# Kernel tuning notes

Measured on AMD Instinct MI355X. Metric: run time of the kernel, lower is better.

Reference implementation:

```python
import jax, jax.numpy as jnp
import numpy as np

D_MODEL = 256; D_FFN = 1024; N_LEVELS = 4; N_HEADS = 8; N_POINTS = 4; N_VT = 8
D_HEAD = D_MODEL // N_HEADS
SHAPES = [(64, 64), (32, 32), (16, 16), (8, 8)]
L_SP = sum(h * w for h, w in SHAPES)  # 5440
BATCH = 4
EPS = 1e-5


def _ln(x, g, b):
    m = jnp.mean(x, -1, keepdims=True)
    xc = x - m
    v = jnp.mean(xc * xc, -1, keepdims=True)
    return g * xc * jax.lax.rsqrt(v + EPS) + b


def _bilinear(v_flat, x, y, H, W):
    # v_flat: (N, H*W, M, Dh); x, y: (N, Q, M) pixel coords (align_corners=False, zero padding)
    x0 = jnp.floor(x); y0 = jnp.floor(y)
    wx = x - x0; wy = y - y0
    out = 0.0
    for cx, cy, w in ((x0, y0, (1 - wx) * (1 - wy)), (x0 + 1, y0, wx * (1 - wy)),
                      (x0, y0 + 1, (1 - wx) * wy), (x0 + 1, y0 + 1, wx * wy)):
        valid = (cx >= 0) & (cx < W) & (cy >= 0) & (cy < H)
        xi = jnp.clip(cx, 0, W - 1).astype(jnp.int32)
        yi = jnp.clip(cy, 0, H - 1).astype(jnp.int32)
        idx = (yi * W + xi)[..., None]  # (N, Q, M, 1)
        g = jnp.take_along_axis(v_flat, idx, axis=1)  # (N, Q, M, Dh)
        out = out + (w * valid)[..., None] * g
    return out


def _msdeform_attn(query, ref, value_in, shapes_np, pad_mask, Wv, bv, Wo, bo, Wa, ba, Wp, bp):
    N, Lq, D = query.shape
    M, Lv, P, Dh = N_HEADS, N_LEVELS, N_POINTS, D_HEAD
    value = value_in @ Wv.T + bv
    value = jnp.where(pad_mask[..., None], 0.0, value)
    value = value.reshape(N, Lq, M, Dh)
    off = (query @ Wo.T + bo).reshape(N, Lq, M, Lv, P, 2)
    attn = jax.nn.softmax((query @ Wa.T + ba).reshape(N, Lq, M, Lv * P), axis=-1)
    attn = attn.reshape(N, Lq, M, Lv, P)
    # offset normalizer is (W, H) per level
    normalizer = jnp.asarray([[w, h] for h, w in shapes_np], jnp.float32)
    loc = ref[:, :, None, :, None, :] + off / normalizer[None, None, None, :, None, :]
    out = 0.0
    start = 0
    for l, (H, W) in enumerate(shapes_np):
        v_l = value[:, start:start + H * W]  # (N, H*W, M, Dh)
        x = (loc[:, :, :, l, :, 0] * W - 0.5).transpose(0, 1, 3, 2).reshape(N, Lq * P, M)
        y = (loc[:, :, :, l, :, 1] * H - 0.5).transpose(0, 1, 3, 2).reshape(N, Lq * P, M)
        samp = _bilinear(v_l, x, y, H, W).reshape(N, Lq, P, M, Dh)
        out = out + jnp.einsum('nqpmd,nqmp->nqmd', samp, attn[:, :, :, l, :])
        start += H * W
    return out.reshape(N, Lq, D) @ Wp.T + bp


def setup_inputs() -> dict:
    key = jax.random.key(0)
    ks = jax.random.split(key, 16)
    N, D = BATCH, D_MODEL
    Lq = L_SP + N_VT
    s = D ** -0.5
    rn = lambda k, sh, sc=1.0: jax.random.normal(k, sh, dtype=jnp.float32) * sc
    starts = np.cumsum([0] + [h * w for h, w in SHAPES[:-1]])
    return {
        'src': rn(ks[0], (N, L_SP, D)),
        'pos': rn(ks[1], (N, L_SP, D), 0.1),
        'reference_points': jax.random.uniform(ks[2], (N, Lq, N_LEVELS, 2), dtype=jnp.float32),
        'spatial_shapes': jnp.asarray(SHAPES, jnp.int32),
        'level_start_index': jnp.asarray(starts, jnp.int32),
        'padding_mask': jnp.zeros((N, Lq), bool),
        'all_vt': rn(ks[3], (N, 75 * N_VT, D)),
        'sel_vt': rn(ks[4], (N, N_VT, D)),
        'W_value': rn(ks[5], (D, D), s), 'b_value': jnp.zeros((D,), jnp.float32),
        'W_off': rn(ks[6], (N_HEADS * N_LEVELS * N_POINTS * 2, D), s),
        'b_off': rn(ks[7], (N_HEADS * N_LEVELS * N_POINTS * 2,), 0.1),
        'W_attn': rn(ks[8], (N_HEADS * N_LEVELS * N_POINTS, D), s),
        'b_attn': jnp.zeros((N_HEADS * N_LEVELS * N_POINTS,), jnp.float32),
        'W_out': rn(ks[9], (D, D), s), 'b_out': jnp.zeros((D,), jnp.float32),
        'g1': jnp.ones((D,), jnp.float32), 'beta1': jnp.zeros((D,), jnp.float32),
        'W1': rn(ks[10], (D_FFN, D), s), 'bf1': jnp.zeros((D_FFN,), jnp.float32),
        'W2': rn(ks[11], (D, D_FFN), D_FFN ** -0.5), 'bf2': jnp.zeros((D,), jnp.float32),
        'g2': jnp.ones((D,), jnp.float32), 'beta2': jnp.zeros((D,), jnp.float32),
    }


def reference(src, pos, reference_points, spatial_shapes, level_start_index, padding_mask,
              all_vt, sel_vt, W_value, b_value, W_off, b_off, W_attn, b_attn, W_out, b_out,
              g1, beta1, W1, bf1, W2, bf2, g2, beta2):
    shapes_np = [tuple(int(v) for v in row) for row in np.asarray(spatial_shapes)]
    q = jnp.concatenate([src + pos, sel_vt], axis=1)      # (N, Lq, D)
    v_in = jnp.concatenate([src, sel_vt], axis=1)
    src2 = _msdeform_attn(q, reference_points, v_in, shapes_np, padding_mask,
                          W_value, b_value, W_off, b_off, W_attn, b_attn, W_out, b_out)
    x = _ln(v_in + src2, g1, beta1)
    h = jax.nn.relu(x @ W1.T + bf1) @ W2.T + bf2
    x = _ln(x + h, g2, beta2)
    return (x[:, :L_SP, :], all_vt, x[:, L_SP:, :])
```

## Files before the change

kernel.cpp:

```cpp
#include <hip/hip_runtime.h>
#include <math.h>

#define NB   4
#define LQ   5448
#define LSP  5440
#define NR   21792
#define DM   256

typedef unsigned short u16;
typedef __attribute__((ext_vector_type(8))) short short8;
typedef __attribute__((ext_vector_type(4))) float f32x4;
typedef __attribute__((ext_vector_type(4))) unsigned int uint4v;

__device__ __forceinline__ u16 f2bf(float f) {
  unsigned int u = __float_as_uint(f);
  u = (u + 0x7fff + ((u >> 16) & 1)) >> 16;
  return (u16)u;
}
__device__ __forceinline__ float bf2f(u16 u) {
  return __uint_as_float(((unsigned int)u) << 16);
}
__device__ __forceinline__ uint4v pack8(float4 a, float4 b) {
  uint4v r;
  r.x = (unsigned)f2bf(a.x) | ((unsigned)f2bf(a.y) << 16);
  r.y = (unsigned)f2bf(a.z) | ((unsigned)f2bf(a.w) << 16);
  r.z = (unsigned)f2bf(b.x) | ((unsigned)f2bf(b.y) << 16);
  r.w = (unsigned)f2bf(b.z) | ((unsigned)f2bf(b.w) << 16);
  return r;
}

#define OFF_R0 0ull
#define OFF_R1 44630016ull
#define OFF_R2 55787520ull
#define OFF_R3 66945024ull
#define OFF_WB 78102528ull
#define OFF_BI 79609856ull

#define WOF_V  0
#define WOF_OA 65536
#define WOF_P  163840
#define WOF_1  229376
#define WOF_2  491520
#define NWELEM 753664

#define OUT0 5570560ull
#define OUT1 614400ull

__global__ __launch_bounds__(256) void convw_k(
    const float* __restrict__ Wv, const float* __restrict__ Wo,
    const float* __restrict__ Wa, const float* __restrict__ Wp,
    const float* __restrict__ W1, const float* __restrict__ W2,
    const float* __restrict__ bo, const float* __restrict__ ba,
    u16* __restrict__ out, float* __restrict__ boa)
{
  const int gid = blockIdx.x * 256 + threadIdx.x;
  if (gid < 384) boa[gid] = (gid < 256) ? bo[gid] : ba[gid - 256];
  if (gid >= NWELEM) return;
  float v;
  if (gid < WOF_OA) {
    v = Wv[gid];
  } else if (gid < WOF_P) {
    const int o = gid - WOF_OA;
    v = (o < 65536) ? Wo[o] : Wa[o - 65536];
  } else if (gid < WOF_1) {
    v = Wp[gid - WOF_P];
  } else if (gid < WOF_2) {
    v = W1[gid - WOF_1];
  } else {
    v = W2[gid - WOF_2];
  }
  out[gid] = f2bf(v);
}

template <int AMODE, int EPI, int BN, int NITER>
__global__ __launch_bounds__(BN) void gemmP(
    const u16* __restrict__ A, int lda,
    const float* __restrict__ src, const float* __restrict__ pos,
    const float* __restrict__ sel,
    const u16* __restrict__ B, int ldb,
    const float* __restrict__ bias, int K,
    u16* __restrict__ outb, int ldob,
    const u16* __restrict__ xbf,
    const float* __restrict__ gvec, const float* __restrict__ bvec,
    float* __restrict__ outf, int ldof)
{
  constexpr int NW = BN / 64;
  __shared__ u16 As[32 * 256];
  __shared__ u16 Bs[NW * 4096];
  const int tid = threadIdx.x;
  const int w = tid >> 6, lane = tid & 63;
  const int l15 = lane & 15, quad = lane >> 4;
  const int m0 = blockIdx.y * 32;
  const int n0 = blockIdx.x * (BN * NITER);
  const int swz = (quad ^ ((l15 >> 1) & 3)) * 8;

  const int rA = (tid & 127) >> 2;
  const int pA = tid & 3;
  const int jb = ((tid >> 7) & 1) * 4;
  const int cA = (pA ^ ((rA >> 1) & 3)) * 8;
  const int ldsA = rA * 32 + pA * 8;
  int gmA = m0 + rA; if (gmA >= NR) gmA = NR - 1;
  const float* aV = nullptr; const float* aP = nullptr;
  if (AMODE) {
    const int n = gmA / LQ, i = gmA - n * LQ;
    if (i < LSP) {
      aV = src + ((size_t)(n * LSP + i)) * DM;
      if (AMODE == 1) aP = pos + ((size_t)(n * LSP + i)) * DM;
    } else {
      aV = sel + ((size_t)(n * 8 + (i - LSP))) * DM;
    }
  }

  int rB[4], cB[4], lB[4];
#pragma unroll
  for (int i = 0; i < 4; ++i) {
    const int g = lane + i * 64;
    rB[i] = g >> 2;
    const int p = g & 3;
    cB[i] = (p ^ ((rB[i] >> 1) & 3)) * 8;
    lB[i] = w * 4096 + rB[i] * 32 + p * 8;
  }

  for (int it = 0; it < NITER; ++it) {
    const u16* Brow = B + (size_t)(n0 + it * BN + w * 64) * ldb;
    f32x4 acc[2][4] = {};

    for (int kc = 0; kc < K; kc += 256) {
      if (NITER == 1 || it == 0) {
        if (kc) __syncthreads();
        if (tid < 256) {
          if (AMODE == 0) {
            const u16* ap = A + (size_t)gmA * lda + kc + cA;
            uint4v t0 = *(const uint4v*)(ap + (jb + 0) * 32);
            uint4v t1 = *(const uint4v*)(ap + (jb + 1) * 32);
            uint4v t2 = *(const uint4v*)(ap + (jb + 2) * 32);
            uint4v t3 = *(const uint4v*)(ap + (jb + 3) * 32);
            *(uint4v*)&As[(jb + 0) * 1024 + ldsA] = t0;
            *(uint4v*)&As[(jb + 1) * 1024 + ldsA] = t1;
            *(uint4v*)&As[(jb + 2) * 1024 + ldsA] = t2;
            *(uint4v*)&As[(jb + 3) * 1024 + ldsA] = t3;
          } else {
#pragma unroll
            for (int i = 0; i < 4; i += 2) {
              const int j0 = jb + i, j1 = jb + i + 1;
              float4 v0a = *(const float4*)(aV + kc + j0 * 32 + cA);
              float4 v0b = *(const float4*)(aV + kc + j0 * 32 + cA + 4);
              float4 v1a = *(const float4*)(aV + kc + j1 * 32 + cA);
              float4 v1b = *(const float4*)(aV + kc + j1 * 32 + cA + 4);
              if (AMODE == 1 && aP) {
                const float4 p0a = *(const float4*)(aP + kc + j0 * 32 + cA);
                const float4 p0b = *(const float4*)(aP + kc + j0 * 32 + cA + 4);
                const float4 p1a = *(const float4*)(aP + kc + j1 * 32 + cA);
                const float4 p1b = *(const float4*)(aP + kc + j1 * 32 + cA + 4);
                v0a.x += p0a.x; v0a.y += p0a.y; v0a.z += p0a.z; v0a.w += p0a.w;
                v0b.x += p0b.x; v0b.y += p0b.y; v0b.z += p0b.z; v0b.w += p0b.w;
                v1a.x += p1a.x; v1a.y += p1a.y; v1a.z += p1a.z; v1a.w += p1a.w;
                v1b.x += p1b.x; v1b.y += p1b.y; v1b.z += p1b.z; v1b.w += p1b.w;
              }
              *(uint4v*)&As[j0 * 1024 + ldsA] = pack8(v0a, v0b);
              *(uint4v*)&As[j1 * 1024 + ldsA] = pack8(v1a, v1b);
            }
          }
        }
        __syncthreads();
      }

      uint4v rb0[4], rb1[4];
#pragma unroll
      for (int i = 0; i < 4; ++i)
        rb0[i] = *(const uint4v*)(Brow + (size_t)rB[i] * ldb + kc + cB[i]);
#pragma unroll
      for (int i = 0; i < 4; ++i)
        rb1[i] = *(const uint4v*)(Brow + (size_t)rB[i] * ldb + kc + 32 + cB[i]);
#pragma unroll
      for (int i = 0; i < 4; ++i) *(uint4v*)&Bs[lB[i]] = rb0[i];

#pragma unroll
      for (int j = 0; j < 8; ++j) {
        if (j < 6) {
          if ((j & 1) == 0) {
#pragma unroll
            for (int i = 0; i < 4; ++i)
              rb0[i] = *(const uint4v*)(Brow + (size_t)rB[i] * ldb + kc + (j + 2) * 32 + cB[i]);
          } else {
#pragma unroll
            for (int i = 0; i < 4; ++i)
              rb1[i] = *(const uint4v*)(Brow + (size_t)rB[i] * ldb + kc + (j + 2) * 32 + cB[i]);
          }
        }
        short8 af[2], bfr[4];
#pragma unroll
        for (int r = 0; r < 2; ++r)
          af[r] = *(const short8*)&As[j * 1024 + (r * 16 + l15) * 32 + swz];
#pragma unroll
        for (int c = 0; c < 4; ++c)
          bfr[c] = *(const short8*)&Bs[w * 4096 + (j & 1) * 2048 + (c * 16 + l15) * 32 + swz];
        if (j < 7) {
          const int buf = ((j + 1) & 1) * 2048;
          if ((j & 1) == 0) {
#pragma unroll
            for (int i = 0; i < 4; ++i) *(uint4v*)&Bs[lB[i] + buf] = rb1[i];
          } else {
#pragma unroll
            for (int i = 0; i < 4; ++i) *(uint4v*)&Bs[lB[i] + buf] = rb0[i];
          }
        }
        __builtin_amdgcn_s_setprio(1);
#pragma unroll
        for (int r = 0; r < 2; ++r)
#pragma unroll
          for (int c = 0; c < 4; ++c)
            acc[r][c] = __builtin_amdgcn_mfma_f32_16x16x32_bf16(af[r], bfr[c], acc[r][c], 0, 0, 0);
        __builtin_amdgcn_s_setprio(0);
      }
    }

    int col[4];
    float bb[4];
#pragma unroll
    for (int c = 0; c < 4; ++c) {
      col[c] = n0 + it * BN + w * 64 + c * 16 + l15;
      bb[c] = bias[col[c]];
    }

    if (EPI == 4) {
#pragma unroll
      for (int c = 0; c < 4; ++c)
#pragma unroll
        for (int r = 0; r < 2; ++r)
#pragma unroll
          for (int j = 0; j < 4; ++j) {
            const int row = m0 + r * 16 + quad * 4 + j;
            if (row < NR) outf[(size_t)row * ldof + col[c]] = acc[r][c][j] + bb[c];
          }
      continue;
    }

    if (EPI <= 1) {
#pragma unroll
      for (int c = 0; c < 4; ++c)
#pragma unroll
        for (int r = 0; r < 2; ++r)
#pragma unroll
          for (int j = 0; j < 4; ++j) {
            const int row = m0 + r * 16 + quad * 4 + j;
            if (row < NR) {
              float v = acc[r][c][j] + bb[c];
              if (EPI == 1) v = fmaxf(v, 0.f);
              outb[(size_t)row * ldob + col[c]] = f2bf(v);
            }
          }
      continue;
    }

    __syncthreads();
    float sv[2][4], sq[2][4];
#pragma unroll
    for (int r = 0; r < 2; ++r) {
#pragma unroll
      for (int j = 0; j < 4; ++j) {
        const int row = m0 + r * 16 + quad * 4 + j;
        const int rc = (row < NR) ? row : NR - 1;
        if (EPI == 2) {
          const int n = rc / LQ;
          const int i = rc - n * LQ;
          const float* resb = (i < LSP)
              ? src + ((size_t)(n * LSP + i)) * DM
              : sel + ((size_t)(n * 8 + (i - LSP))) * DM;
#pragma unroll
          for (int c = 0; c < 4; ++c) acc[r][c][j] += bb[c] + resb[col[c]];
        } else {
#pragma unroll
          for (int c = 0; c < 4; ++c)
            acc[r][c][j] += bb[c] + bf2f(xbf[(size_t)rc * DM + col[c]]);
        }
        float s = 0.f, q = 0.f;
#pragma unroll
        for (int c = 0; c < 4; ++c) {
          const float v = acc[r][c][j];
          s += v; q += v * v;
        }
        sv[r][j] = s; sq[r][j] = q;
      }
    }
#pragma unroll
    for (int off = 1; off < 16; off <<= 1) {
#pragma unroll
      for (int r = 0; r < 2; ++r)
#pragma unroll
        for (int j = 0; j < 4; ++j) {
          sv[r][j] += __shfl_xor(sv[r][j], off, 64);
          sq[r][j] += __shfl_xor(sq[r][j], off, 64);
        }
    }
    float* red = (float*)As;
    if (l15 == 0) {
#pragma unroll
      for (int r = 0; r < 2; ++r)
#pragma unroll
        for (int j = 0; j < 4; ++j) {
          const int rl = r * 16 + quad * 4 + j;
          red[(rl * 4 + w) * 2 + 0] = sv[r][j];
          red[(rl * 4 + w) * 2 + 1] = sq[r][j];
        }
    }
    __syncthreads();

    float gg[4], b2[4];
#pragma unroll
    for (int c = 0; c < 4; ++c) { gg[c] = gvec[col[c]]; b2[c] = bvec[col[c]]; }

#pragma unroll
    for (int r = 0; r < 2; ++r) {
#pragma unroll
      for (int j = 0; j < 4; ++j) {
        const int row = m0 + r * 16 + quad * 4 + j;
        if (row >= NR) continue;
        const int rl = r * 16 + quad * 4 + j;
        float ms = 0.f, mq = 0.f;
#pragma unroll
        for (int ww = 0; ww < 4; ++ww) {
          ms += red[(rl * 4 + ww) * 2 + 0];
          mq += red[(rl * 4 + ww) * 2 + 1];
        }
        const float mean = ms * (1.f / 256.f);
        const float var = mq * (1.f / 256.f) - mean * mean;
        const float rin = rsqrtf(var + 1e-5f);
        if (EPI == 2) {
#pragma unroll
          for (int c = 0; c < 4; ++c)
            outb[(size_t)row * DM + col[c]] =
                f2bf(gg[c] * (acc[r][c][j] - mean) * rin + b2[c]);
        } else {
          const int n = row / LQ;
          const int i = row - n * LQ;
          float* dst = (i < LSP)
              ? outf + (size_t)(n * LSP + i) * DM
              : outf + OUT0 + OUT1 + (size_t)(n * 8 + (i - LSP)) * DM;
#pragma unroll
          for (int c = 0; c < 4; ++c)
            dst[col[c]] = gg[c] * (acc[r][c][j] - mean) * rin + b2[c];
        }
      }
    }
  }
}

__device__ __forceinline__ void fma8(float* a, const uint4v u, float w) {
  a[0] += w * __uint_as_float(u.x << 16);
  a[1] += w * __uint_as_float(u.x & 0xffff0000u);
  a[2] += w * __uint_as_float(u.y << 16);
  a[3] += w * __uint_as_float(u.y & 0xffff0000u);
  a[4] += w * __uint_as_float(u.z << 16);
  a[5] += w * __uint_as_float(u.z & 0xffff0000u);
  a[6] += w * __uint_as_float(u.w << 16);
  a[7] += w * __uint_as_float(u.w & 0xffff0000u);
}

__global__ __launch_bounds__(256) void sample4_k(
    const u16* __restrict__ value, const float* __restrict__ oa,
    const float* __restrict__ ref, u16* __restrict__ samp)
{
  const int lb = blockIdx.x;
  const int xcd = lb & 7;
  const int idx = lb >> 3;
  const int batch = xcd >> 1;
  const int rg = idx * 2 + (xcd & 1);
  const int lane = threadIdx.x & 63;
  const int hi = lane >> 5;
  const int li = lane & 31;
  const int m = li >> 2, q4 = li & 3;
  const int row = batch * LQ + rg * 4 + (threadIdx.x >> 6);

  const float* oar = oa + (size_t)row * 384;
  const float* offm = oar + m * 32;

  const float4 lg = *(const float4*)(oar + 256 + m * 16 + q4 * 4);
  float mx = fmaxf(fmaxf(lg.x, lg.y), fmaxf(lg.z, lg.w));
  mx = fmaxf(mx, __shfl_xor(mx, 1, 64));
  mx = fmaxf(mx, __shfl_xor(mx, 2, 64));
  const float e0 = __expf(lg.x - mx), e1 = __expf(lg.y - mx),
              e2 = __expf(lg.z - mx), e3 = __expf(lg.w - mx);
  float s = e0 + e1 + e2 + e3;
  s += __shfl_xor(s, 1, 64);
  s += __shfl_xor(s, 2, 64);
  const float inv = 1.f / s;
  float wp[4] = {e0 * inv, e1 * inv, e2 * inv, e3 * inv};

  const int L0 = hi * 2;
  float aw[2][4];
#pragma unroll
  for (int p = 0; p < 4; ++p) {
#pragma unroll
    for (int t = 0; t < 2; ++t)
      aw[t][p] = __shfl(wp[p], (lane & ~3) | (L0 + t), 64);
  }

  const float4 r01 = *(const float4*)(ref + (size_t)row * 8);
  const float4 r23 = *(const float4*)(ref + (size_t)row * 8 + 4);
  const float RXa[4] = {r01.x, r01.z, r23.x, r23.z};
  const float RYa[4] = {r01.y, r01.w, r23.y, r23.w};
  const int HW[4] = {64, 32, 16, 8};
  const int ST[4] = {0, 4096, 5120, 5376};

  float a[8] = {};
#pragma unroll
  for (int t = 0; t < 2; ++t) {
    const int l = L0 + t;
    const int W = HW[l];
    const float rx = RXa[l], ry = RYa[l];
    const u16* vb = value + ((size_t)(batch * LQ + ST[l])) * DM + m * 32 + q4 * 8;
    const float4 oA = *(const float4*)(offm + l * 8);
    const float4 oB = *(const float4*)(offm + l * 8 + 4);
    const float ox[4] = {oA.x, oA.z, oB.x, oB.z};
    const float oy[4] = {oA.y, oA.w, oB.y, oB.w};
#pragma unroll
    for (int p = 0; p < 4; ++p) {
      const float px = rx * (float)W + ox[p] - 0.5f;
      const float py = ry * (float)W + oy[p] - 0.5f;
      const float xf = floorf(px), yf = floorf(py);
      const float wx = px - xf, wy = py - yf;
      const int x0 = (int)xf, y0 = (int)yf;
      const int x1 = x0 + 1, y1 = y0 + 1;
      const float vx0 = ((x0 >= 0) & (x0 < W)) ? 1.f : 0.f;
      const float vx1 = ((x1 >= 0) & (x1 < W)) ? 1.f : 0.f;
      const float vy0 = ((y0 >= 0) & (y0 < W)) ? 1.f : 0.f;
      const float vy1 = ((y1 >= 0) & (y1 < W)) ? 1.f : 0.f;
      const int cx0 = min(max(x0, 0), W - 1), cx1 = min(max(x1, 0), W - 1);
      const int cy0 = min(max(y0, 0), W - 1), cy1 = min(max(y1, 0), W - 1);
      const float awp = aw[t][p];
      const float w00 = awp * (1.f - wx) * (1.f - wy) * vx0 * vy0;
      const float w01 = awp * wx * (1.f - wy) * vx1 * vy0;
      const float w10 = awp * (1.f - wx) * wy * vx0 * vy1;
      const float w11 = awp * wx * wy * vx1 * vy1;
      const uint4v v00 = *(const uint4v*)(vb + (size_t)(cy0 * W + cx0) * DM);
      const uint4v v01 = *(const uint4v*)(vb + (size_t)(cy0 * W + cx1) * DM);
      const uint4v v10 = *(const uint4v*)(vb + (size_t)(cy1 * W + cx0) * DM);
      const uint4v v11 = *(const uint4v*)(vb + (size_t)(cy1 * W + cx1) * DM);
      fma8(a, v00, w00);
      fma8(a, v01, w01);
      fma8(a, v10, w10);
      fma8(a, v11, w11);
    }
  }
#pragma unroll
  for (int i = 0; i < 8; ++i) a[i] += __shfl_xor(a[i], 32, 64);

  if (hi == 0) {
    uint4v ov;
    ov.x = (unsigned int)f2bf(a[0]) | ((unsigned int)f2bf(a[1]) << 16);
    ov.y = (unsigned int)f2bf(a[2]) | ((unsigned int)f2bf(a[3]) << 16);
    ov.z = (unsigned int)f2bf(a[4]) | ((unsigned int)f2bf(a[5]) << 16);
    ov.w = (unsigned int)f2bf(a[6]) | ((unsigned int)f2bf(a[7]) << 16);
    *(uint4v*)(samp + (size_t)row * DM + m * 32 + q4 * 8) = ov;
  }
}

extern "C" void kernel_launch(void* const* d_in, const int* in_sizes, int n_in,
                              void* d_out, int out_size, void* d_ws, size_t ws_size,
                              hipStream_t stream)
{
  const float* src = (const float*)d_in[0];
  const float* pos = (const float*)d_in[1];
  const float* ref = (const float*)d_in[2];
  const float* all_vt = (const float*)d_in[6];
  const float* sel = (const float*)d_in[7];
  const float* Wv = (const float*)d_in[8];
  const float* bv = (const float*)d_in[9];
  const float* Wo = (const float*)d_in[10];
  const float* bo = (const float*)d_in[11];
  const float* Wa = (const float*)d_in[12];
  const float* ba = (const float*)d_in[13];
  const float* Wp = (const float*)d_in[14];
  const float* bp = (const float*)d_in[15];
  const float* g1 = (const float*)d_in[16];
  const float* be1 = (const float*)d_in[17];
  const float* W1 = (const float*)d_in[18];
  const float* b1 = (const float*)d_in[19];
  const float* W2 = (const float*)d_in[20];
  const float* b2 = (const float*)d_in[21];
  const float* g2 = (const float*)d_in[22];
  const float* be2 = (const float*)d_in[23];

  char* ws = (char*)d_ws;
  float* oabuf = (float*)(ws + OFF_R0);
  u16* h_bf    = (u16*)(ws + OFF_R0);
  u16* samp_bf = (u16*)(ws + OFF_R1);
  u16* x_bf    = (u16*)(ws + OFF_R2);
  u16* val_bf  = (u16*)(ws + OFF_R3);
  u16* WB      = (u16*)(ws + OFF_WB);
  float* boa   = (float*)(ws + OFF_BI);

  const dim3 b256(256), b384(384);
  const int MT32 = (NR + 31) / 32;

  convw_k<<<dim3(NWELEM / 256), b256, 0, stream>>>(
      Wv, Wo, Wa, Wp, W1, W2, bo, ba, WB, boa);
  gemmP<2, 0, 256, 1><<<dim3(1, MT32), b256, 0, stream>>>(
      nullptr, 0, src, nullptr, sel, WB + WOF_V, 256, bv, 256,
      val_bf, 256, nullptr, nullptr, nullptr, nullptr, 0);
  gemmP<1, 4, 384, 1><<<dim3(1, MT32), b384, 0, stream>>>(
      nullptr, 0, src, pos, sel, WB + WOF_OA, 256, boa, 256,
      nullptr, 0, nullptr, nullptr, nullptr, oabuf, 384);
  sample4_k<<<dim3(8 * 681), b256, 0, stream>>>(val_bf, oabuf, ref, samp_bf);
  gemmP<0, 2, 256, 1><<<dim3(1, MT32), b256, 0, stream>>>(
      samp_bf, 256, src, nullptr, sel, WB + WOF_P, 256, bp, 256,
      x_bf, 256, nullptr, g1, be1, nullptr, 0);
  gemmP<0, 1, 256, 2><<<dim3(2, MT32), b256, 0, stream>>>(
      x_bf, 256, nullptr, nullptr, nullptr, WB + WOF_1, 256, b1, 256,
      h_bf, 1024, nullptr, nullptr, nullptr, nullptr, 0);
  gemmP<0, 3, 256, 1><<<dim3(1, MT32), b256, 0, stream>>>(
      h_bf, 1024, nullptr, nullptr, nullptr, WB + WOF_2, 1024, b2, 1024,
      nullptr, 0, x_bf, g2, be2, (float*)d_out, 0);
  hipMemcpyAsync((float*)d_out + OUT0, all_vt, OUT1 * sizeof(float),
                 hipMemcpyDeviceToDevice, stream);
}
```

Baseline: 296.0 us.

## Parameterize GEMM row tile, use 16-row tiles and single-buffered B staging

Adds a BM template parameter so every GEMM launch uses 16-row tiles instead of 32. This doubles the block count to fill the GPU's CUs better and shrinks LDS use. The per-warp B tile in LDS goes from double- to single-buffered, and the s_setprio hints around the MFMAs are removed. The FFN1 GEMM now launches four column blocks with NITER=1 instead of looping. The cost is less reuse of the weight tile per block, roughly doubling weight reads from L2, and less overlap between B staging and compute.

After: 330.7 us. 11.7% more time.

```diff
diff --git a/kernel.cpp b/kernel.cpp
--- a/kernel.cpp
+++ b/kernel.cpp
@@ -72,7 +72,7 @@
   out[gid] = f2bf(v);
 }
 
-template <int AMODE, int EPI, int BN, int NITER>
+template <int AMODE, int EPI, int BM, int BN, int NITER>
 __global__ __launch_bounds__(BN) void gemmP(
     const u16* __restrict__ A, int lda,
     const float* __restrict__ src, const float* __restrict__ pos,
@@ -85,18 +85,23 @@
     float* __restrict__ outf, int ldof)
 {
   constexpr int NW = BN / 64;
-  __shared__ u16 As[32 * 256];
-  __shared__ u16 Bs[NW * 4096];
+  constexpr int MR = BM / 16;
+  constexpr int TS = BM * 32;
+  constexpr int SL = BM * 4;
+  constexpr int NG = 256 / SL;
+  constexpr int TPG = 8 / NG;
+  __shared__ u16 As[BM * 256];
+  __shared__ u16 Bs[NW * 2048];
   const int tid = threadIdx.x;
   const int w = tid >> 6, lane = tid & 63;
   const int l15 = lane & 15, quad = lane >> 4;
-  const int m0 = blockIdx.y * 32;
+  const int m0 = blockIdx.y * BM;
   const int n0 = blockIdx.x * (BN * NITER);
   const int swz = (quad ^ ((l15 >> 1) & 3)) * 8;
 
-  const int rA = (tid & 127) >> 2;
+  const int rA = (tid & (SL - 1)) >> 2;
   const int pA = tid & 3;
-  const int jb = ((tid >> 7) & 1) * 4;
+  const int jb = ((tid / SL) & (NG - 1)) * TPG;
   const int cA = (pA ^ ((rA >> 1) & 3)) * 8;
   const int ldsA = rA * 32 + pA * 8;
   int gmA = m0 + rA; if (gmA >= NR) gmA = NR - 1;
@@ -118,12 +123,12 @@
     rB[i] = g >> 2;
     const int p = g & 3;
     cB[i] = (p ^ ((rB[i] >> 1) & 3)) * 8;
-    lB[i] = w * 4096 + rB[i] * 32 + p * 8;
+    lB[i] = w * 2048 + rB[i] * 32 + p * 8;
   }
 
   for (int it = 0; it < NITER; ++it) {
     const u16* Brow = B + (size_t)(n0 + it * BN + w * 64) * ldb;
-    f32x4 acc[2][4] = {};
+    f32x4 acc[MR][4] = {};
 
     for (int kc = 0; kc < K; kc += 256) {
       if (NITER == 1 || it == 0) {
@@ -131,17 +136,14 @@
         if (tid < 256) {
           if (AMODE == 0) {
             const u16* ap = A + (size_t)gmA * lda + kc + cA;
-            uint4v t0 = *(const uint4v*)(ap + (jb + 0) * 32);
-            uint4v t1 = *(const uint4v*)(ap + (jb + 1) * 32);
-            uint4v t2 = *(const uint4v*)(ap + (jb + 2) * 32);
-            uint4v t3 = *(const uint4v*)(ap + (jb + 3) * 32);
-            *(uint4v*)&As[(jb + 0) * 1024 + ldsA] = t0;
-            *(uint4v*)&As[(jb + 1) * 1024 + ldsA] = t1;
-            *(uint4v*)&As[(jb + 2) * 1024 + ldsA] = t2;
-            *(uint4v*)&As[(jb + 3) * 1024 + ldsA] = t3;
+#pragma unroll
+            for (int t = 0; t < TPG; ++t) {
+              const uint4v tt = *(const uint4v*)(ap + (jb + t) * 32);
+              *(uint4v*)&As[(jb + t) * TS + ldsA] = tt;
+            }
           } else {
 #pragma unroll
-            for (int i = 0; i < 4; i += 2) {
+            for (int i = 0; i < TPG; i += 2) {
               const int j0 = jb + i, j1 = jb + i + 1;
               float4 v0a = *(const float4*)(aV + kc + j0 * 32 + cA);
               float4 v0b = *(const float4*)(aV + kc + j0 * 32 + cA + 4);
@@ -157,8 +159,8 @@
                 v1a.x += p1a.x; v1a.y += p1a.y; v1a.z += p1a.z; v1a.w += p1a.w;
                 v1b.x += p1b.x; v1b.y += p1b.y; v1b.z += p1b.z; v1b.w += p1b.w;
               }
-              *(uint4v*)&As[j0 * 1024 + ldsA] = pack8(v0a, v0b);
-              *(uint4v*)&As[j1 * 1024 + ldsA] = pack8(v1a, v1b);
+              *(uint4v*)&As[j0 * TS + ldsA] = pack8(v0a, v0b);
+              *(uint4v*)&As[j1 * TS + ldsA] = pack8(v1a, v1b);
             }
           }
         }
@@ -170,13 +172,29 @@
       for (int i = 0; i < 4; ++i)
         rb0[i] = *(const uint4v*)(Brow + (size_t)rB[i] * ldb + kc + cB[i]);
 #pragma unroll
+      for (int i = 0; i < 4; ++i) *(uint4v*)&Bs[lB[i]] = rb0[i];
+#pragma unroll
       for (int i = 0; i < 4; ++i)
         rb1[i] = *(const uint4v*)(Brow + (size_t)rB[i] * ldb + kc + 32 + cB[i]);
-#pragma unroll
-      for (int i = 0; i < 4; ++i) *(uint4v*)&Bs[lB[i]] = rb0[i];
 
 #pragma unroll
       for (int j = 0; j < 8; ++j) {
+        short8 af[MR], bfr[4];
+#pragma unroll
+        for (int r = 0; r < MR; ++r)
+          af[r] = *(const short8*)&As[j * TS + (r * 16 + l15) * 32 + swz];
+#pragma unroll
+        for (int c = 0; c < 4; ++c)
+          bfr[c] = *(const short8*)&Bs[w * 2048 + (c * 16 + l15) * 32 + swz];
+        if (j < 7) {
+          if ((j & 1) == 0) {
+#pragma unroll
+            for (int i = 0; i < 4; ++i) *(uint4v*)&Bs[lB[i]] = rb1[i];
+          } else {
+#pragma unroll
+            for (int i = 0; i < 4; ++i) *(uint4v*)&Bs[lB[i]] = rb0[i];
+          }
+        }
         if (j < 6) {
           if ((j & 1) == 0) {
 #pragma unroll
@@ -188,30 +206,11 @@
               rb1[i] = *(const uint4v*)(Brow + (size_t)rB[i] * ldb + kc + (j + 2) * 32 + cB[i]);
           }
         }
-        short8 af[2], bfr[4];
-#pragma unroll
-        for (int r = 0; r < 2; ++r)
-          af[r] = *(const short8*)&As[j * 1024 + (r * 16 + l15) * 32 + swz];
-#pragma unroll
-        for (int c = 0; c < 4; ++c)
-          bfr[c] = *(const short8*)&Bs[w * 4096 + (j & 1) * 2048 + (c * 16 + l15) * 32 + swz];
-        if (j < 7) {
-          const int buf = ((j + 1) & 1) * 2048;
-          if ((j & 1) == 0) {
-#pragma unroll
-            for (int i = 0; i < 4; ++i) *(uint4v*)&Bs[lB[i] + buf] = rb1[i];
-          } else {
-#pragma unroll
-            for (int i = 0; i < 4; ++i) *(uint4v*)&Bs[lB[i] + buf] = rb0[i];
-          }
-        }
-        __builtin_amdgcn_s_setprio(1);
-#pragma unroll
-        for (int r = 0; r < 2; ++r)
+#pragma unroll
+        for (int r = 0; r < MR; ++r)
 #pragma unroll
           for (int c = 0; c < 4; ++c)
             acc[r][c] = __builtin_amdgcn_mfma_f32_16x16x32_bf16(af[r], bfr[c], acc[r][c], 0, 0, 0);
-        __builtin_amdgcn_s_setprio(0);
       }
     }
 
@@ -227,7 +226,7 @@
 #pragma unroll
       for (int c = 0; c < 4; ++c)
 #pragma unroll
-        for (int r = 0; r < 2; ++r)
+        for (int r = 0; r < MR; ++r)
 #pragma unroll
           for (int j = 0; j < 4; ++j) {
             const int row = m0 + r * 16 + quad * 4 + j;
@@ -240,7 +239,7 @@
 #pragma unroll
       for (int c = 0; c < 4; ++c)
 #pragma unroll
-        for (int r = 0; r < 2; ++r)
+        for (int r = 0; r < MR; ++r)
 #pragma unroll
           for (int j = 0; j < 4; ++j) {
             const int row = m0 + r * 16 + quad * 4 + j;
@@ -254,9 +253,9 @@
     }
 
     __syncthreads();
-    float sv[2][4], sq[2][4];
-#pragma unroll
-    for (int r = 0; r < 2; ++r) {
+    float sv[MR][4], sq[MR][4];
+#pragma unroll
+    for (int r = 0; r < MR; ++r) {
 #pragma unroll
       for (int j = 0; j < 4; ++j) {
         const int row = m0 + r * 16 + quad * 4 + j;
@@ -286,7 +285,7 @@
 #pragma unroll
     for (int off = 1; off < 16; off <<= 1) {
 #pragma unroll
-      for (int r = 0; r < 2; ++r)
+      for (int r = 0; r < MR; ++r)
 #pragma unroll
         for (int j = 0; j < 4; ++j) {
           sv[r][j] += __shfl_xor(sv[r][j], off, 64);
@@ -296,12 +295,12 @@
     float* red = (float*)As;
     if (l15 == 0) {
 #pragma unroll
-      for (int r = 0; r < 2; ++r)
+      for (int r = 0; r < MR; ++r)
 #pragma unroll
         for (int j = 0; j < 4; ++j) {
           const int rl = r * 16 + quad * 4 + j;
-          red[(rl * 4 + w) * 2 + 0] = sv[r][j];
-          red[(rl * 4 + w) * 2 + 1] = sq[r][j];
+          red[(rl * NW + w) * 2 + 0] = sv[r][j];
+          red[(rl * NW + w) * 2 + 1] = sq[r][j];
         }
     }
     __syncthreads();
@@ -311,7 +310,7 @@
     for (int c = 0; c < 4; ++c) { gg[c] = gvec[col[c]]; b2[c] = bvec[col[c]]; }
 
 #pragma unroll
-    for (int r = 0; r < 2; ++r) {
+    for (int r = 0; r < MR; ++r) {
 #pragma unroll
       for (int j = 0; j < 4; ++j) {
         const int row = m0 + r * 16 + quad * 4 + j;
@@ -319,9 +318,9 @@
         const int rl = r * 16 + quad * 4 + j;
         float ms = 0.f, mq = 0.f;
 #pragma unroll
-        for (int ww = 0; ww < 4; ++ww) {
-          ms += red[(rl * 4 + ww) * 2 + 0];
-          mq += red[(rl * 4 + ww) * 2 + 1];
+        for (int ww = 0; ww < NW; ++ww) {
+          ms += red[(rl * NW + ww) * 2 + 0];
+          mq += red[(rl * NW + ww) * 2 + 1];
         }
         const float mean = ms * (1.f / 256.f);
         const float var = mq * (1.f / 256.f) - mean * mean;
@@ -492,24 +491,24 @@
   float* boa   = (float*)(ws + OFF_BI);
 
   const dim3 b256(256), b384(384);
-  const int MT32 = (NR + 31) / 32;
+  const int MT16 = NR / 16;
 
   convw_k<<<dim3(NWELEM / 256), b256, 0, stream>>>(
       Wv, Wo, Wa, Wp, W1, W2, bo, ba, WB, boa);
-  gemmP<2, 0, 256, 1><<<dim3(1, MT32), b256, 0, stream>>>(
+  gemmP<2, 0, 16, 256, 1><<<dim3(1, MT16), b256, 0, stream>>>(
       nullptr, 0, src, nullptr, sel, WB + WOF_V, 256, bv, 256,
       val_bf, 256, nullptr, nullptr, nullptr, nullptr, 0);
-  gemmP<1, 4, 384, 1><<<dim3(1, MT32), b384, 0, stream>>>(
+  gemmP<1, 4, 16, 384, 1><<<dim3(1, MT16), b384, 0, stream>>>(
       nullptr, 0, src, pos, sel, WB + WOF_OA, 256, boa, 256,
       nullptr, 0, nullptr, nullptr, nullptr, oabuf, 384);
   sample4_k<<<dim3(8 * 681), b256, 0, stream>>>(val_bf, oabuf, ref, samp_bf);
-  gemmP<0, 2, 256, 1><<<dim3(1, MT32), b256, 0, stream>>>(
+  gemmP<0, 2, 16, 256, 1><<<dim3(1, MT16), b256, 0, stream>>>(
       samp_bf, 256, src, nullptr, sel, WB + WOF_P, 256, bp, 256,
       x_bf, 256, nullptr, g1, be1, nullptr, 0);
-  gemmP<0, 1, 256, 2><<<dim3(2, MT32), b256, 0, stream>>>(
+  gemmP<0, 1, 16, 256, 1><<<dim3(4, MT16), b256, 0, stream>>>(
       x_bf, 256, nullptr, nullptr, nullptr, WB + WOF_1, 256, b1, 256,
       h_bf, 1024, nullptr, nullptr, nullptr, nullptr, 0);
-  gemmP<0, 3, 256, 1><<<dim3(1, MT32), b256, 0, stream>>>(
+  gemmP<0, 3, 16, 256, 1><<<dim3(1, MT16), b256, 0, stream>>>(
       h_bf, 1024, nullptr, nullptr, nullptr, WB + WOF_2, 1024, b2, 1024,
       nullptr, 0, x_bf, g2, be2, (float*)d_out, 0);
   hipMemcpyAsync((float*)d_out + OUT0, all_vt, OUT1 * sizeof(float),
```
